# Optimization experiments

Hardware: AMD Instinct MI355X
Metric: run time of the kernel (lower is better)

Reference implementation:

```python
import jax, jax.numpy as jnp
import numpy as np

N = 50000
E = 800000
NUM_IDS = 2048
IN_CH = 16
HID = 32
HEADS = 4
EMB = 8
GAT_IN = EMB + (IN_CH - 1)  # 23
NEG_SLOPE = 0.2


def gat_layer(x, src, dst, W, a_src, a_dst, b):
    """PyG-style GATConv (self-loops already appended to src/dst).
    x: [N, Fin]; W: [Fin, H*C]; a_src/a_dst: [H, C]; b: [H*C].
    Returns [N, H*C] (heads concatenated)."""
    H, C = a_src.shape
    h = (x @ W).reshape(-1, H, C)                      # [N,H,C]
    alpha_s = jnp.sum(h * a_src, axis=-1)              # [N,H]
    alpha_d = jnp.sum(h * a_dst, axis=-1)              # [N,H]
    e = jax.nn.leaky_relu(alpha_s[src] + alpha_d[dst], NEG_SLOPE)  # [E',H]
    # segment softmax over destination neighborhoods
    m = jax.ops.segment_max(e, dst, num_segments=N)    # [N,H]
    ex = jnp.exp(e - m[dst])
    denom = jax.ops.segment_sum(ex, dst, num_segments=N)
    alpha = ex / (denom[dst] + 1e-16)                  # [E',H]
    msg = h[src] * alpha[:, :, None]                   # [E',H,C]
    out = jax.ops.segment_sum(msg, dst, num_segments=N)  # [N,H,C]
    return out.reshape(-1, H * C) + b


def setup_inputs() -> dict:
    key = jax.random.key(0)
    ks = jax.random.split(key, 20)
    node_ids = jax.random.randint(ks[0], (N,), 0, NUM_IDS, dtype=jnp.int32)
    node_feats = jax.random.normal(ks[1], (N, IN_CH - 1), dtype=jnp.float32)
    src = jax.random.randint(ks[2], (E,), 0, N, dtype=jnp.int32)
    off = jax.random.randint(ks[3], (E,), 1, N, dtype=jnp.int32)
    dst = (src + off) % N  # guarantee no pre-existing self-loops
    edge_index = jnp.stack([src, dst]).astype(jnp.int32)
    batch = jnp.zeros((N,), dtype=jnp.int32)

    def w(k, shape):
        return jax.random.normal(k, shape, dtype=jnp.float32) * 0.1

    emb = w(ks[4], (NUM_IDS, EMB))
    # enc1: GAT_IN -> HID, heads=HEADS
    W1, a1s, a1d, b1 = w(ks[5], (GAT_IN, HEADS * HID)), w(ks[6], (HEADS, HID)), w(ks[7], (HEADS, HID)), jnp.zeros((HEADS * HID,), jnp.float32)
    # enc2: HID*HEADS -> HID, heads=1
    W2, a2s, a2d, b2 = w(ks[8], (HEADS * HID, HID)), w(ks[9], (1, HID)), w(ks[10], (1, HID)), jnp.zeros((HID,), jnp.float32)
    # dec1: HID -> HID, heads=HEADS
    W3, a3s, a3d, b3 = w(ks[11], (HID, HEADS * HID)), w(ks[12], (HEADS, HID)), w(ks[13], (HEADS, HID)), jnp.zeros((HEADS * HID,), jnp.float32)
    # dec2: HID*HEADS -> IN_CH, heads=1
    W4, a4s, a4d, b4 = w(ks[14], (HEADS * HID, IN_CH)), w(ks[15], (1, IN_CH)), w(ks[16], (1, IN_CH)), jnp.zeros((IN_CH,), jnp.float32)
    return {"node_ids": node_ids, "node_feats": node_feats, "edge_index": edge_index,
            "batch": batch, "emb": emb,
            "W1": W1, "a1s": a1s, "a1d": a1d, "b1": b1,
            "W2": W2, "a2s": a2s, "a2d": a2d, "b2": b2,
            "W3": W3, "a3s": a3s, "a3d": a3d, "b3": b3,
            "W4": W4, "a4s": a4s, "a4d": a4d, "b4": b4}


def reference(node_ids, node_feats, edge_index, batch, emb,
              W1, a1s, a1d, b1, W2, a2s, a2d, b2,
              W3, a3s, a3d, b3, W4, a4s, a4d, b4):
    # PyG GATConv adds self-loops by default
    loop = jnp.arange(N, dtype=edge_index.dtype)
    src = jnp.concatenate([edge_index[0], loop])
    dst = jnp.concatenate([edge_index[1], loop])
    x = jnp.concatenate([emb[node_ids], node_feats], axis=1)  # [N, GAT_IN]
    x = jax.nn.relu(gat_layer(x, src, dst, W1, a1s, a1d, b1))
    x = jax.nn.relu(gat_layer(x, src, dst, W2, a2s, a2d, b2))
    x = jax.nn.relu(gat_layer(x, src, dst, W3, a3s, a3d, b3))
    x = jax.nn.sigmoid(gat_layer(x, src, dst, W4, a4s, a4d, b4))
    return x
```

## Files before the change

### kernel.cpp

```cpp
#include <hip/hip_runtime.h>
#include <hip/hip_bf16.h>

typedef __hip_bfloat16 bf16;
typedef float f32x2 __attribute__((ext_vector_type(2)));

#define NEG_SLOPE 0.2f
#define DCAP 128

__device__ __forceinline__ float lrelu(float x) { return fmaxf(x, NEG_SLOPE * x); }
__device__ __forceinline__ f32x2 bfp(unsigned pv) {
    f32x2 r;
    r.x = __uint_as_float(pv << 16);
    r.y = __uint_as_float(pv & 0xffff0000u);
    return r;
}
__device__ __forceinline__ void fma8p(f32x2* acc, float w, uint4 pv) {
    f32x2 wv = {w, w};
    acc[0] += wv * bfp(pv.x);
    acc[1] += wv * bfp(pv.y);
    acc[2] += wv * bfp(pv.z);
    acc[3] += wv * bfp(pv.w);
}
__device__ __forceinline__ ushort bfbits(float x) {
    bf16 b = __float2bfloat16(x);
    return *reinterpret_cast<ushort*>(&b);
}

static inline int cdiv(int a, int b) { return (a + b - 1) / b; }
__host__ __device__ static inline int imin(int a, int b) { return a < b ? a : b; }

__global__ void fill_sentinel(float* __restrict__ y, int n) {
    int t = blockIdx.x * 256 + threadIdx.x;
    if (t < n) y[t] = 2.0f;
}

__global__ __launch_bounds__(256) void init_and_t1(
    int* __restrict__ cursor, int IB,
    const int* __restrict__ ids, const float* __restrict__ feats,
    const float* __restrict__ emb, const float* __restrict__ W1,
    const float* __restrict__ a1s, const float* __restrict__ a1d,
    bf16* __restrict__ h_out, float* __restrict__ as_out, float* __restrict__ ad_out, int N) {
    if ((int)blockIdx.x < IB) {
        int i = blockIdx.x * 256 + threadIdx.x;
        if (i < N) cursor[i] = i * DCAP;
        return;
    }
    constexpr int FIN = 23, FINP = 27, HC = 128;
    __shared__ float xs[2 * FINP];
    __shared__ __align__(16) float w1_s[FIN * HC];
    const int node0 = (blockIdx.x - IB) * 2;
    const int tid = threadIdx.x;
    for (int i = tid; i < FIN * HC / 4; i += 256)
        ((float4*)w1_s)[i] = ((const float4*)W1)[i];
    if (tid < 2 * FIN) {
        int ln = tid / FIN, f = tid - ln * FIN;
        int i = node0 + ln;
        float v = 0.f;
        if (i < N) v = (f < 8) ? emb[ids[i] * 8 + f] : feats[i * 15 + (f - 8)];
        xs[ln * FINP + f] = v;
    }
    __syncthreads();
    const int ln = tid >> 7, j = tid & 127;
    const int i = node0 + ln;
    if (i >= N) return;
    float acc = 0.f;
#pragma unroll
    for (int f = 0; f < FIN; ++f) acc += xs[ln * FINP + f] * w1_s[f * HC + j];
    h_out[(size_t)i * HC + j] = __float2bfloat16(acc);
    float s = acc * a1s[j];
    float d = acc * a1d[j];
#pragma unroll
    for (int off = 16; off > 0; off >>= 1) {
        s += __shfl_down(s, off, 32);
        d += __shfl_down(d, off, 32);
    }
    if ((j & 31) == 0) {
        as_out[i * 4 + j / 32] = s;
        ad_out[i * 4 + j / 32] = d;
    }
}

template <typename EIDX>
__global__ void fill_direct(const int* __restrict__ src, const int* __restrict__ dst,
                            int* __restrict__ cursor, EIDX* __restrict__ elsrc, int E) {
    int t = blockIdx.x * 256 + threadIdx.x;
    if (t >= E) return;
    int d = dst[t];
    int slot = atomicAdd(&cursor[d], 1);
    if (slot < d * DCAP + DCAP) elsrc[slot] = (EIDX)src[t];
}

template <int H, int C, int HN, int CN, bool FINAL, typename EIDX>
__global__ __launch_bounds__(256) void gat_tf(
    const int* __restrict__ cursor, const EIDX* __restrict__ elsrc,
    const bf16* __restrict__ hIn, const float* __restrict__ asIn,
    const float* __restrict__ adIn, const float* __restrict__ bias,
    const float* __restrict__ Wn, const float* __restrict__ anS,
    const float* __restrict__ anD, bf16* __restrict__ hOut,
    float* __restrict__ asOut, float* __restrict__ adOut,
    float* __restrict__ yout, int N) {
    constexpr int HC = H * C;
    constexpr int HCN = HN * CN;
    constexpr int LPR = HC / 8;
    constexpr int EPI = 64 / LPR;
    constexpr int HCP = HC + 4;
    __shared__ int src_s[256];
    __shared__ float w_s[256 * H];
    __shared__ float xs[FINAL ? 1 : 4 * HCP];
    __shared__ __align__(16) float wn_s[FINAL ? 4 : HC * HCN];
    __shared__ __align__(16) float an_s[FINAL ? 4 : 2 * HCN];
    __shared__ float bias_s[HC];
    const int tid = threadIdx.x;
    if constexpr (!FINAL) {
        for (int i = tid; i < HC * HCN / 4; i += 256)
            ((float4*)wn_s)[i] = ((const float4*)Wn)[i];
        if (tid < HCN) {
            an_s[tid] = anS[tid];
            an_s[HCN + tid] = anD[tid];
        }
    }
    if (tid < HC) bias_s[tid] = bias[tid];
    __syncthreads();

    const int wvi = tid >> 6;
    const int lane = tid & 63;
    const int d = blockIdx.x * 4 + wvi;
    if (d >= N) return;
    const int grp = lane / LPR;
    const int lin = lane - grp * LPR;
    const int ch0 = 8 * lin;
    const int h0 = ch0 / C;

    {
        const int row = d * DCAP;
        const int s_pre = (int)elsrc[row + lane];
        const int end = imin(cursor[d], row + DCAP);
        float ad_d[H], c[H], den_p[H];
        if constexpr (H == 4) {
            float4 adv = *(const float4*)(adIn + d * 4);
            float4 asv = *(const float4*)(asIn + d * 4);
            ad_d[0] = adv.x; ad_d[1] = adv.y; ad_d[2] = adv.z; ad_d[3] = adv.w;
            c[0] = lrelu(asv.x + adv.x);
            c[1] = lrelu(asv.y + adv.y);
            c[2] = lrelu(asv.z + adv.z);
            c[3] = lrelu(asv.w + adv.w);
            den_p[0] = den_p[1] = den_p[2] = den_p[3] = 0.f;
        } else {
            ad_d[0] = adIn[d];
            c[0] = lrelu(asIn[d] + ad_d[0]);
            den_p[0] = 0.f;
        }
        f32x2 acc[4];
#pragma unroll
        for (int q = 0; q < 4; ++q) acc[q] = (f32x2){0.f, 0.f};
        if (grp == 0) {
            uint4 pv = *(const uint4*)(hIn + (size_t)d * HC + ch0);
            acc[0] = bfp(pv.x);
            acc[1] = bfp(pv.y);
            acc[2] = bfp(pv.z);
            acc[3] = bfp(pv.w);
        }
        for (int base = row; base < end; base += 64) {
            int e = base + lane;
            int s = (base == row) ? s_pre : ((e < end) ? (int)elsrc[e] : -1);
            if (e >= end) s = -1;
            if constexpr (H == 4) {
                float4 w4 = {0.f, 0.f, 0.f, 0.f};
                if (s >= 0) {
                    float4 av = *(const float4*)(asIn + s * 4);
                    w4.x = __expf(lrelu(av.x + ad_d[0]) - c[0]);
                    w4.y = __expf(lrelu(av.y + ad_d[1]) - c[1]);
                    w4.z = __expf(lrelu(av.z + ad_d[2]) - c[2]);
                    w4.w = __expf(lrelu(av.w + ad_d[3]) - c[3]);
                    den_p[0] += w4.x;
                    den_p[1] += w4.y;
                    den_p[2] += w4.z;
                    den_p[3] += w4.w;
                }
                *(float4*)&w_s[(wvi * 64 + lane) * 4] = w4;
            } else {
                float w0 = 0.f;
                if (s >= 0) {
                    w0 = __expf(lrelu(asIn[s] + ad_d[0]) - c[0]);
                    den_p[0] += w0;
                }
                w_s[wvi * 64 + lane] = w0;
            }
            src_s[wvi * 64 + lane] = (s >= 0) ? s : 0;
            int nv = imin(64, end - base);
#pragma unroll 4
            for (int k0 = 0; k0 < nv; k0 += EPI) {
                int k = k0 + grp;
                if (k < nv) {
                    int sk = src_s[wvi * 64 + k];
                    float w = w_s[(wvi * 64 + k) * H + h0];
                    uint4 pv = *(const uint4*)(hIn + (size_t)sk * HC + ch0);
                    fma8p(acc, w, pv);
                }
            }
        }
#pragma unroll
        for (int h = 0; h < H; ++h) {
            float v = den_p[h];
#pragma unroll
            for (int o = 32; o > 0; o >>= 1) v += __shfl_xor(v, o, 64);
            den_p[h] = v + 1.0f;
        }
#pragma unroll
        for (int o = LPR; o < 64; o <<= 1) {
#pragma unroll
            for (int q = 0; q < 4; ++q) {
                acc[q].x += __shfl_xor(acc[q].x, o, 64);
                acc[q].y += __shfl_xor(acc[q].y, o, 64);
            }
        }
        if (grp == 0) {
            float inv = 1.f / (den_p[h0] + 1e-16f);
            float v[8];
#pragma unroll
            for (int q = 0; q < 4; ++q) {
                v[2 * q] = acc[q].x * inv + bias_s[ch0 + 2 * q];
                v[2 * q + 1] = acc[q].y * inv + bias_s[ch0 + 2 * q + 1];
            }
            if constexpr (FINAL) {
                float4 o0, o1;
                o0.x = 1.f / (1.f + __expf(-v[0]));
                o0.y = 1.f / (1.f + __expf(-v[1]));
                o0.z = 1.f / (1.f + __expf(-v[2]));
                o0.w = 1.f / (1.f + __expf(-v[3]));
                o1.x = 1.f / (1.f + __expf(-v[4]));
                o1.y = 1.f / (1.f + __expf(-v[5]));
                o1.z = 1.f / (1.f + __expf(-v[6]));
                o1.w = 1.f / (1.f + __expf(-v[7]));
                *(float4*)(yout + (size_t)d * HC + ch0) = o0;
                *(float4*)(yout + (size_t)d * HC + ch0 + 4) = o1;
            } else {
#pragma unroll
                for (int r = 0; r < 8; ++r)
                    xs[wvi * HCP + ch0 + r] = v[r] > 0.f ? v[r] : 0.f;
            }
        }
    }

    if constexpr (!FINAL) {
        __builtin_amdgcn_wave_barrier();
        const float* xrow = xs + wvi * HCP;
        constexpr int PJ = HCN / 2;
        constexpr int SEG = 64 / PJ;
        constexpr int FSEG = HC / SEG;
        constexpr int PPH = CN / 2;
        const int jp = lane % PJ;
        const int seg = lane / PJ;
        const int f0 = seg * FSEG;
        float a0 = 0.f, a1 = 0.f;
#pragma unroll
        for (int f = 0; f < FSEG; f += 4) {
            float4 xv = *(const float4*)&xrow[f0 + f];
            float2 w0 = *(const float2*)&wn_s[(f0 + f + 0) * HCN + 2 * jp];
            float2 w1 = *(const float2*)&wn_s[(f0 + f + 1) * HCN + 2 * jp];
            float2 w2 = *(const float2*)&wn_s[(f0 + f + 2) * HCN + 2 * jp];
            float2 w3 = *(const float2*)&wn_s[(f0 + f + 3) * HCN + 2 * jp];
            a0 += xv.x * w0.x + xv.y * w1.x + xv.z * w2.x + xv.w * w3.x;
            a1 += xv.x * w0.y + xv.y * w1.y + xv.z * w2.y + xv.w * w3.y;
        }
#pragma unroll
        for (int o = PJ; o < 64; o <<= 1) {
            a0 += __shfl_xor(a0, o, 64);
            a1 += __shfl_xor(a1, o, 64);
        }
        if (seg == 0) {
            ushort2 st;
            st.x = bfbits(a0);
            st.y = bfbits(a1);
            *(ushort2*)(hOut + (size_t)d * HCN + 2 * jp) = st;
        }
        float2 aS = *(const float2*)&an_s[2 * jp];
        float2 aD = *(const float2*)&an_s[HCN + 2 * jp];
        float sv = a0 * aS.x + a1 * aS.y;
        float dv = a0 * aD.x + a1 * aD.y;
#pragma unroll
        for (int o = PPH / 2; o > 0; o >>= 1) {
            sv += __shfl_down(sv, o, PPH);
            dv += __shfl_down(dv, o, PPH);
        }
        if (seg == 0 && (jp % PPH) == 0) {
            asOut[d * HN + jp / PPH] = sv;
            adOut[d * HN + jp / PPH] = dv;
        }
    }
}

template <typename EIDX>
static void run_layers(const int* cursor, const EIDX* elsrc, bf16* hA, bf16* hB,
                       float* asA, float* adA, float* asB, float* adB, float* y,
                       void* const* d_in, int N, hipStream_t stream) {
    const float* b1 = (const float*)d_in[8];
    const float* W2 = (const float*)d_in[9];
    const float* a2s = (const float*)d_in[10];
    const float* a2d = (const float*)d_in[11];
    const float* b2 = (const float*)d_in[12];
    const float* W3 = (const float*)d_in[13];
    const float* a3s = (const float*)d_in[14];
    const float* a3d = (const float*)d_in[15];
    const float* b3 = (const float*)d_in[16];
    const float* W4 = (const float*)d_in[17];
    const float* a4s = (const float*)d_in[18];
    const float* a4d = (const float*)d_in[19];
    const float* b4 = (const float*)d_in[20];
    const int g = cdiv(N, 4);
    gat_tf<4, 32, 1, 32, false, EIDX><<<g, 256, 0, stream>>>(
        cursor, elsrc, hA, asA, adA, b1, W2, a2s, a2d, hB, asB, adB, y, N);
    gat_tf<1, 32, 4, 32, false, EIDX><<<g, 256, 0, stream>>>(
        cursor, elsrc, hB, asB, adB, b2, W3, a3s, a3d, hA, asA, adA, y, N);
    gat_tf<4, 32, 1, 16, false, EIDX><<<g, 256, 0, stream>>>(
        cursor, elsrc, hA, asA, adA, b3, W4, a4s, a4d, hB, asB, adB, y, N);
    gat_tf<1, 16, 1, 1, true, EIDX><<<g, 256, 0, stream>>>(
        cursor, elsrc, hB, asB, adB, b4, W4, a4s, a4d, hA, asA, adA, y, N);
}

extern "C" void kernel_launch(void* const* d_in, const int* in_sizes, int n_in,
                              void* d_out, int out_size, void* d_ws, size_t ws_size,
                              hipStream_t stream) {
    const int N = in_sizes[0];
    const int E = in_sizes[2] / 2;
    const int* node_ids = (const int*)d_in[0];
    const float* feats = (const float*)d_in[1];
    const int* srcI = (const int*)d_in[2];
    const int* dstI = srcI + E;
    const float* emb = (const float*)d_in[4];
    const float* W1 = (const float*)d_in[5];
    const float* a1s = (const float*)d_in[6];
    const float* a1d = (const float*)d_in[7];
    float* y = (float*)d_out;

    float* asA = (float*)d_ws;
    float* adA = asA + (size_t)N * 4;
    float* asB = adA + (size_t)N * 4;
    float* adB = asB + (size_t)N * 4;
    bf16* hA = (bf16*)(adB + (size_t)N * 4);
    bf16* hB = hA + (size_t)N * 128;
    int* cursor = (int*)(hB + (size_t)N * 128);
    int* elsrc = cursor + N;

    const bool u16 = (N <= 65536);
    size_t elsz = (size_t)N * DCAP * (u16 ? 2 : 4);
    size_t need = (size_t)N * 4 * 4 * 4 + (size_t)N * 128 * 2 * 2 + (size_t)N * 4 + elsz;
    if (ws_size < need) {
        fill_sentinel<<<cdiv(out_size, 256), 256, 0, stream>>>(y, out_size);
        return;
    }

    const int IB = cdiv(N, 256);
    init_and_t1<<<IB + cdiv(N, 2), 256, 0, stream>>>(cursor, IB, node_ids, feats, emb,
                                                     W1, a1s, a1d, hA, asA, adA, N);
    if (u16) {
        ushort* el16 = (ushort*)elsrc;
        fill_direct<ushort><<<cdiv(E, 256), 256, 0, stream>>>(srcI, dstI, cursor, el16, E);
        run_layers<ushort>(cursor, el16, hA, hB, asA, adA, asB, adB, y, d_in, N, stream);
    } else {
        fill_direct<int><<<cdiv(E, 256), 256, 0, stream>>>(srcI, dstI, cursor, elsrc, E);
        run_layers<int>(cursor, elsrc, hA, hB, asA, adA, asB, adB, y, d_in, N, stream);
    }
}
```

Before: 380.0 us.

## Enlarge blocks to 1024 threads and read layer weights from global instead of LDS

```diff
diff --git a/kernel.cpp b/kernel.cpp
--- a/kernel.cpp
+++ b/kernel.cpp
@@ -34,26 +34,26 @@
     if (t < n) y[t] = 2.0f;
 }
 
-__global__ __launch_bounds__(256) void init_and_t1(
+__global__ __launch_bounds__(1024) void init_and_t1(
     int* __restrict__ cursor, int IB,
     const int* __restrict__ ids, const float* __restrict__ feats,
     const float* __restrict__ emb, const float* __restrict__ W1,
     const float* __restrict__ a1s, const float* __restrict__ a1d,
     bf16* __restrict__ h_out, float* __restrict__ as_out, float* __restrict__ ad_out, int N) {
     if ((int)blockIdx.x < IB) {
-        int i = blockIdx.x * 256 + threadIdx.x;
+        int i = blockIdx.x * 1024 + threadIdx.x;
         if (i < N) cursor[i] = i * DCAP;
         return;
     }
     constexpr int FIN = 23, FINP = 27, HC = 128;
-    __shared__ float xs[2 * FINP];
+    __shared__ float xs[8 * FINP];
     __shared__ __align__(16) float w1_s[FIN * HC];
-    const int node0 = (blockIdx.x - IB) * 2;
+    const int node0 = (blockIdx.x - IB) * 8;
     const int tid = threadIdx.x;
-    for (int i = tid; i < FIN * HC / 4; i += 256)
-        ((float4*)w1_s)[i] = ((const float4*)W1)[i];
-    if (tid < 2 * FIN) {
-        int ln = tid / FIN, f = tid - ln * FIN;
+    if (tid < FIN * HC / 4) ((float4*)w1_s)[tid] = ((const float4*)W1)[tid];
+    if (tid >= 1024 - 8 * FIN) {
+        int t2 = tid - (1024 - 8 * FIN);
+        int ln = t2 / FIN, f = t2 - ln * FIN;
         int i = node0 + ln;
         float v = 0.f;
         if (i < N) v = (f < 8) ? emb[ids[i] * 8 + f] : feats[i * 15 + (f - 8)];
@@ -81,9 +81,11 @@
 }
 
 template <typename EIDX>
-__global__ void fill_direct(const int* __restrict__ src, const int* __restrict__ dst,
-                            int* __restrict__ cursor, EIDX* __restrict__ elsrc, int E) {
-    int t = blockIdx.x * 256 + threadIdx.x;
+__global__ __launch_bounds__(1024) void fill_direct(const int* __restrict__ src,
+                                                    const int* __restrict__ dst,
+                                                    int* __restrict__ cursor,
+                                                    EIDX* __restrict__ elsrc, int E) {
+    int t = blockIdx.x * 1024 + threadIdx.x;
     if (t >= E) return;
     int d = dst[t];
     int slot = atomicAdd(&cursor[d], 1);
@@ -91,7 +93,7 @@
 }
 
 template <int H, int C, int HN, int CN, bool FINAL, typename EIDX>
-__global__ __launch_bounds__(256) void gat_tf(
+__global__ __launch_bounds__(1024) void gat_tf(
     const int* __restrict__ cursor, const EIDX* __restrict__ elsrc,
     const bf16* __restrict__ hIn, const float* __restrict__ asIn,
     const float* __restrict__ adIn, const float* __restrict__ bias,
@@ -104,27 +106,13 @@
     constexpr int LPR = HC / 8;
     constexpr int EPI = 64 / LPR;
     constexpr int HCP = HC + 4;
-    __shared__ int src_s[256];
-    __shared__ float w_s[256 * H];
-    __shared__ float xs[FINAL ? 1 : 4 * HCP];
-    __shared__ __align__(16) float wn_s[FINAL ? 4 : HC * HCN];
-    __shared__ __align__(16) float an_s[FINAL ? 4 : 2 * HCN];
-    __shared__ float bias_s[HC];
+    __shared__ int src_s[1024];
+    __shared__ float w_s[1024 * H];
+    __shared__ float xs[FINAL ? 1 : 16 * HCP];
     const int tid = threadIdx.x;
-    if constexpr (!FINAL) {
-        for (int i = tid; i < HC * HCN / 4; i += 256)
-            ((float4*)wn_s)[i] = ((const float4*)Wn)[i];
-        if (tid < HCN) {
-            an_s[tid] = anS[tid];
-            an_s[HCN + tid] = anD[tid];
-        }
-    }
-    if (tid < HC) bias_s[tid] = bias[tid];
-    __syncthreads();
-
     const int wvi = tid >> 6;
     const int lane = tid & 63;
-    const int d = blockIdx.x * 4 + wvi;
+    const int d = blockIdx.x * 16 + wvi;
     if (d >= N) return;
     const int grp = lane / LPR;
     const int lin = lane - grp * LPR;
@@ -219,8 +207,8 @@
             float v[8];
 #pragma unroll
             for (int q = 0; q < 4; ++q) {
-                v[2 * q] = acc[q].x * inv + bias_s[ch0 + 2 * q];
-                v[2 * q + 1] = acc[q].y * inv + bias_s[ch0 + 2 * q + 1];
+                v[2 * q] = acc[q].x * inv + bias[ch0 + 2 * q];
+                v[2 * q + 1] = acc[q].y * inv + bias[ch0 + 2 * q + 1];
             }
             if constexpr (FINAL) {
                 float4 o0, o1;
@@ -256,10 +244,10 @@
 #pragma unroll
         for (int f = 0; f < FSEG; f += 4) {
             float4 xv = *(const float4*)&xrow[f0 + f];
-            float2 w0 = *(const float2*)&wn_s[(f0 + f + 0) * HCN + 2 * jp];
-            float2 w1 = *(const float2*)&wn_s[(f0 + f + 1) * HCN + 2 * jp];
-            float2 w2 = *(const float2*)&wn_s[(f0 + f + 2) * HCN + 2 * jp];
-            float2 w3 = *(const float2*)&wn_s[(f0 + f + 3) * HCN + 2 * jp];
+            float2 w0 = *(const float2*)&Wn[(f0 + f + 0) * HCN + 2 * jp];
+            float2 w1 = *(const float2*)&Wn[(f0 + f + 1) * HCN + 2 * jp];
+            float2 w2 = *(const float2*)&Wn[(f0 + f + 2) * HCN + 2 * jp];
+            float2 w3 = *(const float2*)&Wn[(f0 + f + 3) * HCN + 2 * jp];
             a0 += xv.x * w0.x + xv.y * w1.x + xv.z * w2.x + xv.w * w3.x;
             a1 += xv.x * w0.y + xv.y * w1.y + xv.z * w2.y + xv.w * w3.y;
         }
@@ -274,8 +262,8 @@
             st.y = bfbits(a1);
             *(ushort2*)(hOut + (size_t)d * HCN + 2 * jp) = st;
         }
-        float2 aS = *(const float2*)&an_s[2 * jp];
-        float2 aD = *(const float2*)&an_s[HCN + 2 * jp];
+        float2 aS = *(const float2*)&anS[2 * jp];
+        float2 aD = *(const float2*)&anD[2 * jp];
         float sv = a0 * aS.x + a1 * aS.y;
         float dv = a0 * aD.x + a1 * aD.y;
 #pragma unroll
@@ -307,14 +295,14 @@
     const float* a4s = (const float*)d_in[18];
     const float* a4d = (const float*)d_in[19];
     const float* b4 = (const float*)d_in[20];
-    const int g = cdiv(N, 4);
-    gat_tf<4, 32, 1, 32, false, EIDX><<<g, 256, 0, stream>>>(
+    const int g = cdiv(N, 16);
+    gat_tf<4, 32, 1, 32, false, EIDX><<<g, 1024, 0, stream>>>(
         cursor, elsrc, hA, asA, adA, b1, W2, a2s, a2d, hB, asB, adB, y, N);
-    gat_tf<1, 32, 4, 32, false, EIDX><<<g, 256, 0, stream>>>(
+    gat_tf<1, 32, 4, 32, false, EIDX><<<g, 1024, 0, stream>>>(
         cursor, elsrc, hB, asB, adB, b2, W3, a3s, a3d, hA, asA, adA, y, N);
-    gat_tf<4, 32, 1, 16, false, EIDX><<<g, 256, 0, stream>>>(
+    gat_tf<4, 32, 1, 16, false, EIDX><<<g, 1024, 0, stream>>>(
         cursor, elsrc, hA, asA, adA, b3, W4, a4s, a4d, hB, asB, adB, y, N);
-    gat_tf<1, 16, 1, 1, true, EIDX><<<g, 256, 0, stream>>>(
+    gat_tf<1, 16, 1, 1, true, EIDX><<<g, 1024, 0, stream>>>(
         cursor, elsrc, hB, asB, adB, b4, W4, a4s, a4d, hA, asA, adA, y, N);
 }
 
@@ -350,15 +338,15 @@
         return;
     }
 
-    const int IB = cdiv(N, 256);
-    init_and_t1<<<IB + cdiv(N, 2), 256, 0, stream>>>(cursor, IB, node_ids, feats, emb,
-                                                     W1, a1s, a1d, hA, asA, adA, N);
+    const int IB = cdiv(N, 1024);
+    init_and_t1<<<IB + cdiv(N, 8), 1024, 0, stream>>>(cursor, IB, node_ids, feats, emb,
+                                                      W1, a1s, a1d, hA, asA, adA, N);
     if (u16) {
         ushort* el16 = (ushort*)elsrc;
-        fill_direct<ushort><<<cdiv(E, 256), 256, 0, stream>>>(srcI, dstI, cursor, el16, E);
+        fill_direct<ushort><<<cdiv(E, 1024), 1024, 0, stream>>>(srcI, dstI, cursor, el16, E);
         run_layers<ushort>(cursor, el16, hA, hB, asA, adA, asB, adB, y, d_in, N, stream);
     } else {
-        fill_direct<int><<<cdiv(E, 256), 256, 0, stream>>>(srcI, dstI, cursor, elsrc, E);
+        fill_direct<int><<<cdiv(E, 1024), 1024, 0, stream>>>(srcI, dstI, cursor, elsrc, E);
         run_layers<int>(cursor, elsrc, hA, hB, asA, adA, asB, adB, y, d_in, N, stream);
     }
 }
```

New measurement: 433.1 us. +14.0%, slower.

## Process two destination nodes per wave and read weights from global instead of LDS

Applied to the files above, without the earlier changes.

```diff
diff --git a/kernel.cpp b/kernel.cpp
--- a/kernel.cpp
+++ b/kernel.cpp
@@ -45,14 +45,11 @@
         if (i < N) cursor[i] = i * DCAP;
         return;
     }
-    constexpr int FIN = 23, FINP = 27, HC = 128;
-    __shared__ float xs[2 * FINP];
-    __shared__ __align__(16) float w1_s[FIN * HC];
-    const int node0 = (blockIdx.x - IB) * 2;
+    constexpr int FIN = 23, FINP = 24, HC = 128;
+    __shared__ float xs[8 * FINP];
+    const int node0 = (blockIdx.x - IB) * 8;
     const int tid = threadIdx.x;
-    for (int i = tid; i < FIN * HC / 4; i += 256)
-        ((float4*)w1_s)[i] = ((const float4*)W1)[i];
-    if (tid < 2 * FIN) {
+    if (tid < 8 * FIN) {
         int ln = tid / FIN, f = tid - ln * FIN;
         int i = node0 + ln;
         float v = 0.f;
@@ -60,23 +57,32 @@
         xs[ln * FINP + f] = v;
     }
     __syncthreads();
-    const int ln = tid >> 7, j = tid & 127;
+    const int ln = tid >> 5;
+    const int j0 = (tid & 31) * 4;
     const int i = node0 + ln;
     if (i >= N) return;
-    float acc = 0.f;
-#pragma unroll
-    for (int f = 0; f < FIN; ++f) acc += xs[ln * FINP + f] * w1_s[f * HC + j];
-    h_out[(size_t)i * HC + j] = __float2bfloat16(acc);
-    float s = acc * a1s[j];
-    float d = acc * a1d[j];
-#pragma unroll
-    for (int off = 16; off > 0; off >>= 1) {
-        s += __shfl_down(s, off, 32);
-        d += __shfl_down(d, off, 32);
-    }
-    if ((j & 31) == 0) {
-        as_out[i * 4 + j / 32] = s;
-        ad_out[i * 4 + j / 32] = d;
+    float a0 = 0.f, a1 = 0.f, a2 = 0.f, a3 = 0.f;
+#pragma unroll
+    for (int f = 0; f < FIN; ++f) {
+        float xv = xs[ln * FINP + f];
+        float4 w = *(const float4*)&W1[f * HC + j0];
+        a0 += xv * w.x; a1 += xv * w.y; a2 += xv * w.z; a3 += xv * w.w;
+    }
+    ushort4 st = {bfbits(a0), bfbits(a1), bfbits(a2), bfbits(a3)};
+    *(ushort4*)(h_out + (size_t)i * HC + j0) = st;
+    float4 vs = *(const float4*)&a1s[j0];
+    float4 vd = *(const float4*)&a1d[j0];
+    float s = a0 * vs.x + a1 * vs.y + a2 * vs.z + a3 * vs.w;
+    float d = a0 * vd.x + a1 * vd.y + a2 * vd.z + a3 * vd.w;
+#pragma unroll
+    for (int off = 4; off > 0; off >>= 1) {
+        s += __shfl_down(s, off, 8);
+        d += __shfl_down(d, off, 8);
+    }
+    if ((tid & 7) == 0) {
+        int h = (tid & 31) / 8;
+        as_out[i * 4 + h] = s;
+        ad_out[i * 4 + h] = d;
     }
 }
 
@@ -99,41 +105,31 @@
     const float* __restrict__ anD, bf16* __restrict__ hOut,
     float* __restrict__ asOut, float* __restrict__ adOut,
     float* __restrict__ yout, int N) {
+    constexpr int LG = 32;
     constexpr int HC = H * C;
     constexpr int HCN = HN * CN;
     constexpr int LPR = HC / 8;
-    constexpr int EPI = 64 / LPR;
+    constexpr int EPI = LG / LPR;
     constexpr int HCP = HC + 4;
     __shared__ int src_s[256];
     __shared__ float w_s[256 * H];
-    __shared__ float xs[FINAL ? 1 : 4 * HCP];
-    __shared__ __align__(16) float wn_s[FINAL ? 4 : HC * HCN];
-    __shared__ __align__(16) float an_s[FINAL ? 4 : 2 * HCN];
-    __shared__ float bias_s[HC];
+    __shared__ float xs[FINAL ? 1 : 8 * HCP];
     const int tid = threadIdx.x;
-    if constexpr (!FINAL) {
-        for (int i = tid; i < HC * HCN / 4; i += 256)
-            ((float4*)wn_s)[i] = ((const float4*)Wn)[i];
-        if (tid < HCN) {
-            an_s[tid] = anS[tid];
-            an_s[HCN + tid] = anD[tid];
-        }
-    }
-    if (tid < HC) bias_s[tid] = bias[tid];
-    __syncthreads();
-
     const int wvi = tid >> 6;
     const int lane = tid & 63;
-    const int d = blockIdx.x * 4 + wvi;
-    if (d >= N) return;
-    const int grp = lane / LPR;
-    const int lin = lane - grp * LPR;
+    const int gi = lane >> 5;
+    const int gl = lane & 31;
+    const int d = blockIdx.x * 8 + wvi * 2 + gi;
+    const bool act = d < N;
+    const int grp = gl / LPR;
+    const int lin = gl - grp * LPR;
     const int ch0 = 8 * lin;
     const int h0 = ch0 / C;
-
-    {
+    const int slot0 = wvi * 64 + gi * LG;
+
+    if (act) {
         const int row = d * DCAP;
-        const int s_pre = (int)elsrc[row + lane];
+        const int s_pre = (int)elsrc[row + gl];
         const int end = imin(cursor[d], row + DCAP);
         float ad_d[H], c[H], den_p[H];
         if constexpr (H == 4) {
@@ -160,8 +156,8 @@
             acc[2] = bfp(pv.z);
             acc[3] = bfp(pv.w);
         }
-        for (int base = row; base < end; base += 64) {
-            int e = base + lane;
+        for (int base = row; base < end; base += LG) {
+            int e = base + gl;
             int s = (base == row) ? s_pre : ((e < end) ? (int)elsrc[e] : -1);
             if (e >= end) s = -1;
             if constexpr (H == 4) {
@@ -177,23 +173,23 @@
                     den_p[2] += w4.z;
                     den_p[3] += w4.w;
                 }
-                *(float4*)&w_s[(wvi * 64 + lane) * 4] = w4;
+                *(float4*)&w_s[(slot0 + gl) * 4] = w4;
             } else {
                 float w0 = 0.f;
                 if (s >= 0) {
                     w0 = __expf(lrelu(asIn[s] + ad_d[0]) - c[0]);
                     den_p[0] += w0;
                 }
-                w_s[wvi * 64 + lane] = w0;
-            }
-            src_s[wvi * 64 + lane] = (s >= 0) ? s : 0;
-            int nv = imin(64, end - base);
+                w_s[slot0 + gl] = w0;
+            }
+            src_s[slot0 + gl] = (s >= 0) ? s : 0;
+            int nv = imin(LG, end - base);
 #pragma unroll 4
             for (int k0 = 0; k0 < nv; k0 += EPI) {
                 int k = k0 + grp;
                 if (k < nv) {
-                    int sk = src_s[wvi * 64 + k];
-                    float w = w_s[(wvi * 64 + k) * H + h0];
+                    int sk = src_s[slot0 + k];
+                    float w = w_s[(slot0 + k) * H + h0];
                     uint4 pv = *(const uint4*)(hIn + (size_t)sk * HC + ch0);
                     fma8p(acc, w, pv);
                 }
@@ -203,15 +199,15 @@
         for (int h = 0; h < H; ++h) {
             float v = den_p[h];
 #pragma unroll
-            for (int o = 32; o > 0; o >>= 1) v += __shfl_xor(v, o, 64);
+            for (int o = LG / 2; o > 0; o >>= 1) v += __shfl_xor(v, o, LG);
             den_p[h] = v + 1.0f;
         }
 #pragma unroll
-        for (int o = LPR; o < 64; o <<= 1) {
+        for (int o = LPR; o < LG; o <<= 1) {
 #pragma unroll
             for (int q = 0; q < 4; ++q) {
-                acc[q].x += __shfl_xor(acc[q].x, o, 64);
-                acc[q].y += __shfl_xor(acc[q].y, o, 64);
+                acc[q].x += __shfl_xor(acc[q].x, o, LG);
+                acc[q].y += __shfl_xor(acc[q].y, o, LG);
             }
         }
         if (grp == 0) {
@@ -219,8 +215,8 @@
             float v[8];
 #pragma unroll
             for (int q = 0; q < 4; ++q) {
-                v[2 * q] = acc[q].x * inv + bias_s[ch0 + 2 * q];
-                v[2 * q + 1] = acc[q].y * inv + bias_s[ch0 + 2 * q + 1];
+                v[2 * q] = acc[q].x * inv + bias[ch0 + 2 * q];
+                v[2 * q + 1] = acc[q].y * inv + bias[ch0 + 2 * q + 1];
             }
             if constexpr (FINAL) {
                 float4 o0, o1;
@@ -237,55 +233,93 @@
             } else {
 #pragma unroll
                 for (int r = 0; r < 8; ++r)
-                    xs[wvi * HCP + ch0 + r] = v[r] > 0.f ? v[r] : 0.f;
+                    xs[(wvi * 2 + gi) * HCP + ch0 + r] = v[r] > 0.f ? v[r] : 0.f;
             }
         }
     }
 
     if constexpr (!FINAL) {
         __builtin_amdgcn_wave_barrier();
-        const float* xrow = xs + wvi * HCP;
-        constexpr int PJ = HCN / 2;
-        constexpr int SEG = 64 / PJ;
-        constexpr int FSEG = HC / SEG;
-        constexpr int PPH = CN / 2;
-        const int jp = lane % PJ;
-        const int seg = lane / PJ;
-        const int f0 = seg * FSEG;
-        float a0 = 0.f, a1 = 0.f;
-#pragma unroll
-        for (int f = 0; f < FSEG; f += 4) {
-            float4 xv = *(const float4*)&xrow[f0 + f];
-            float2 w0 = *(const float2*)&wn_s[(f0 + f + 0) * HCN + 2 * jp];
-            float2 w1 = *(const float2*)&wn_s[(f0 + f + 1) * HCN + 2 * jp];
-            float2 w2 = *(const float2*)&wn_s[(f0 + f + 2) * HCN + 2 * jp];
-            float2 w3 = *(const float2*)&wn_s[(f0 + f + 3) * HCN + 2 * jp];
-            a0 += xv.x * w0.x + xv.y * w1.x + xv.z * w2.x + xv.w * w3.x;
-            a1 += xv.x * w0.y + xv.y * w1.y + xv.z * w2.y + xv.w * w3.y;
-        }
-#pragma unroll
-        for (int o = PJ; o < 64; o <<= 1) {
-            a0 += __shfl_xor(a0, o, 64);
-            a1 += __shfl_xor(a1, o, 64);
-        }
-        if (seg == 0) {
-            ushort2 st;
-            st.x = bfbits(a0);
-            st.y = bfbits(a1);
-            *(ushort2*)(hOut + (size_t)d * HCN + 2 * jp) = st;
-        }
-        float2 aS = *(const float2*)&an_s[2 * jp];
-        float2 aD = *(const float2*)&an_s[HCN + 2 * jp];
-        float sv = a0 * aS.x + a1 * aS.y;
-        float dv = a0 * aD.x + a1 * aD.y;
-#pragma unroll
-        for (int o = PPH / 2; o > 0; o >>= 1) {
-            sv += __shfl_down(sv, o, PPH);
-            dv += __shfl_down(dv, o, PPH);
-        }
-        if (seg == 0 && (jp % PPH) == 0) {
-            asOut[d * HN + jp / PPH] = sv;
-            adOut[d * HN + jp / PPH] = dv;
+        if (act) {
+            const float* xrow = xs + (wvi * 2 + gi) * HCP;
+            constexpr int PJ2 = HCN / 2;
+            constexpr int PPH = CN / 2;
+            if constexpr (PJ2 <= LG) {
+                constexpr int SEG = LG / PJ2;
+                constexpr int FSEG = HC / SEG;
+                const int jp = gl % PJ2;
+                const int seg = gl / PJ2;
+                const int f0 = seg * FSEG;
+                float a0 = 0.f, a1 = 0.f;
+#pragma unroll
+                for (int f = 0; f < FSEG; f += 4) {
+                    float4 xv = *(const float4*)&xrow[f0 + f];
+                    float2 w0 = *(const float2*)&Wn[(f0 + f + 0) * HCN + 2 * jp];
+                    float2 w1 = *(const float2*)&Wn[(f0 + f + 1) * HCN + 2 * jp];
+                    float2 w2 = *(const float2*)&Wn[(f0 + f + 2) * HCN + 2 * jp];
+                    float2 w3 = *(const float2*)&Wn[(f0 + f + 3) * HCN + 2 * jp];
+                    a0 += xv.x * w0.x + xv.y * w1.x + xv.z * w2.x + xv.w * w3.x;
+                    a1 += xv.x * w0.y + xv.y * w1.y + xv.z * w2.y + xv.w * w3.y;
+                }
+#pragma unroll
+                for (int o = PJ2; o < LG; o <<= 1) {
+                    a0 += __shfl_xor(a0, o, LG);
+                    a1 += __shfl_xor(a1, o, LG);
+                }
+                if (seg == 0) {
+                    ushort2 st;
+                    st.x = bfbits(a0);
+                    st.y = bfbits(a1);
+                    *(ushort2*)(hOut + (size_t)d * HCN + 2 * jp) = st;
+                }
+                float2 aS = *(const float2*)&anS[2 * jp];
+                float2 aD = *(const float2*)&anD[2 * jp];
+                float sv = a0 * aS.x + a1 * aS.y;
+                float dv = a0 * aD.x + a1 * aD.y;
+#pragma unroll
+                for (int o = PPH / 2; o > 0; o >>= 1) {
+                    sv += __shfl_down(sv, o, PPH);
+                    dv += __shfl_down(dv, o, PPH);
+                }
+                if (seg == 0 && (jp % PPH) == 0) {
+                    asOut[d * HN + jp / PPH] = sv;
+                    adOut[d * HN + jp / PPH] = dv;
+                }
+            } else {
+                constexpr int PPL = PJ2 / LG;
+#pragma unroll
+                for (int p = 0; p < PPL; ++p) {
+                    const int jp = gl + LG * p;
+                    float a0 = 0.f, a1 = 0.f;
+#pragma unroll
+                    for (int f = 0; f < HC; f += 4) {
+                        float4 xv = *(const float4*)&xrow[f];
+                        float2 w0 = *(const float2*)&Wn[(f + 0) * HCN + 2 * jp];
+                        float2 w1 = *(const float2*)&Wn[(f + 1) * HCN + 2 * jp];
+                        float2 w2 = *(const float2*)&Wn[(f + 2) * HCN + 2 * jp];
+                        float2 w3 = *(const float2*)&Wn[(f + 3) * HCN + 2 * jp];
+                        a0 += xv.x * w0.x + xv.y * w1.x + xv.z * w2.x + xv.w * w3.x;
+                        a1 += xv.x * w0.y + xv.y * w1.y + xv.z * w2.y + xv.w * w3.y;
+                    }
+                    ushort2 st;
+                    st.x = bfbits(a0);
+                    st.y = bfbits(a1);
+                    *(ushort2*)(hOut + (size_t)d * HCN + 2 * jp) = st;
+                    float2 aS = *(const float2*)&anS[2 * jp];
+                    float2 aD = *(const float2*)&anD[2 * jp];
+                    float sv = a0 * aS.x + a1 * aS.y;
+                    float dv = a0 * aD.x + a1 * aD.y;
+#pragma unroll
+                    for (int o = PPH / 2; o > 0; o >>= 1) {
+                        sv += __shfl_down(sv, o, PPH);
+                        dv += __shfl_down(dv, o, PPH);
+                    }
+                    if ((jp % PPH) == 0) {
+                        asOut[d * HN + jp / PPH] = sv;
+                        adOut[d * HN + jp / PPH] = dv;
+                    }
+                }
+            }
         }
     }
 }
@@ -307,7 +341,7 @@
     const float* a4s = (const float*)d_in[18];
     const float* a4d = (const float*)d_in[19];
     const float* b4 = (const float*)d_in[20];
-    const int g = cdiv(N, 4);
+    const int g = cdiv(N, 8);
     gat_tf<4, 32, 1, 32, false, EIDX><<<g, 256, 0, stream>>>(
         cursor, elsrc, hA, asA, adA, b1, W2, a2s, a2d, hB, asB, adB, y, N);
     gat_tf<1, 32, 4, 32, false, EIDX><<<g, 256, 0, stream>>>(
@@ -351,7 +385,7 @@
     }
 
     const int IB = cdiv(N, 256);
-    init_and_t1<<<IB + cdiv(N, 2), 256, 0, stream>>>(cursor, IB, node_ids, feats, emb,
+    init_and_t1<<<IB + cdiv(N, 8), 256, 0, stream>>>(cursor, IB, node_ids, feats, emb,
                                                      W1, a1s, a1d, hA, asA, adA, N);
     if (u16) {
         ushort* el16 = (ushort*)elsrc;
```

Result: faster. 357.9 us (-5.8%).
